# Kernel tuning notes

Measured on AMD Instinct MI355X. Metric: run time of the kernel, lower is better.

Reference implementation:

```python
import jax, jax.numpy as jnp
import numpy as np


def setup_inputs() -> dict:
    key = jax.random.key(0)
    ks = jax.random.split(key, 10)
    T, B, I, H, Z = 1024, 512, 128, 256, 1
    s = 0.1  # small init scale for stable recurrence
    return {
        "inputs": jax.random.normal(ks[0], (T, B, I), dtype=jnp.float32),
        "h0": jax.random.normal(ks[1], (B, H), dtype=jnp.float32) * s,
        "c0": jax.random.normal(ks[2], (B, H), dtype=jnp.float32) * s,
        "z0": jax.random.normal(ks[3], (B, Z), dtype=jnp.float32) * s,
        "W_ih": jax.random.normal(ks[4], (4 * H, I + Z), dtype=jnp.float32) * s,
        "W_hh": jax.random.normal(ks[5], (4 * H, H), dtype=jnp.float32) * s,
        "b_ih": jax.random.normal(ks[6], (4 * H,), dtype=jnp.float32) * s,
        "b_hh": jax.random.normal(ks[7], (4 * H,), dtype=jnp.float32) * s,
        "W_fc": jax.random.normal(ks[8], (Z, H), dtype=jnp.float32) * s,
        "b_fc": jax.random.normal(ks[9], (Z,), dtype=jnp.float32) * s,
    }


def reference(inputs, h0, c0, z0, W_ih, W_hh, b_ih, b_hh, W_fc, b_fc):
    def step(carry, x_t):
        h, c, z = carry
        xz = jnp.concatenate([x_t, z], axis=1)  # [B, I+Z]
        gates = xz @ W_ih.T + b_ih + h @ W_hh.T + b_hh  # [B, 4H]
        i_g, f_g, g_g, o_g = jnp.split(gates, 4, axis=1)  # torch gate order i,f,g,o
        i_g = jax.nn.sigmoid(i_g)
        f_g = jax.nn.sigmoid(f_g)
        g_g = jnp.tanh(g_g)
        o_g = jax.nn.sigmoid(o_g)
        c = f_g * c + i_g * g_g
        h = o_g * jnp.tanh(c)
        z = jnp.tanh(h @ W_fc.T + b_fc)  # [B, Z]
        return (h, c, z), z

    (h, c, _), outputs = jax.lax.scan(step, (h0, c0, z0), inputs)
    return outputs, h, c  # outputs: [T, B, Z]
```

## Files before the change

### kernel.cpp

```cpp
#include <hip/hip_runtime.h>
#include <hip/hip_bf16.h>
#include <stdint.h>

#define TT 1024
#define BB 512
#define II 128
#define HH 256
#define NKC 12
#define GSTR 132

typedef __attribute__((ext_vector_type(8))) short bf16x8;
typedef __attribute__((ext_vector_type(4))) float f32x4;
typedef __attribute__((ext_vector_type(4))) uint32_t u32x4;
typedef unsigned long long ull;

__device__ __forceinline__ float fsig(float x)  { return 1.0f / (1.0f + __expf(-x)); }
__device__ __forceinline__ float ftanh(float x) { return 1.0f - 2.0f / (__expf(2.0f * x) + 1.0f); }
__device__ __forceinline__ uint16_t f2bf(float f) {
    return __bfloat16_as_ushort(__float2bfloat16(f));
}
__device__ __forceinline__ float bf2lo(uint32_t w) { return __uint_as_float(w << 16); }
__device__ __forceinline__ float bf2hi(uint32_t w) { return __uint_as_float(w & 0xffff0000u); }

template<int DUAL>
__global__ __launch_bounds__(512, 1) void lstm_kernel(
    const float* __restrict__ x,
    const float* __restrict__ h0, const float* __restrict__ c0,
    const float* __restrict__ z0,
    const float* __restrict__ W_ih, const float* __restrict__ W_hh,
    const float* __restrict__ b_ih, const float* __restrict__ b_hh,
    const float* __restrict__ Wfc, const float* __restrict__ bfc,
    ull* __restrict__ hbF, ull* __restrict__ hbS,
    float* __restrict__ out)
{
    __shared__ __align__(16) uint16_t w_sh[NKC * 8 * 64 * 8];
    __shared__ __align__(16) uint16_t a_sh[NKC * 4 * 16 * 8];
    __shared__ float g_sh[16 * GSTR];
    __shared__ float zp_sh[2][8][16];

    const int tid  = threadIdx.x;
    const int lane = tid & 63, wv = tid >> 6;
    const int bid  = blockIdx.x;
    const int mm   = bid >> 3;
    const int role = mm & 7, grp = (bid & 7) * 4 + (mm >> 3);
    const int b0   = grp * 16;
    const int arow = tid >> 5, auu = tid & 31;
    const int u_g  = role * 32 + auu;
    const int xc   = (tid & 31) * 4;
    const int grole = wv, grow = (tid >> 2) & 15, gwq = tid & 3;

    #pragma unroll
    for (int i = 0; i < 12; ++i) {
        int eo = i * 512 + tid;
        int lane2 = eo & 63, knt = eo >> 6;
        int nt = knt & 7;
        int k0 = (knt >> 3) * 32 + (lane2 >> 4) * 8;
        int lc = nt * 16 + (lane2 & 15);
        int col = (lc >> 5) * 256 + role * 32 + (lc & 31);
        const float* src = (k0 < II) ? &W_ih[(size_t)col * (II + 1) + k0]
                                     : &W_hh[(size_t)col * HH + (k0 - II)];
        ushort4 lo, hi;
        lo.x = f2bf(src[0]); lo.y = f2bf(src[1]); lo.z = f2bf(src[2]); lo.w = f2bf(src[3]);
        hi.x = f2bf(src[4]); hi.y = f2bf(src[5]); hi.z = f2bf(src[6]); hi.w = f2bf(src[7]);
        *(ushort4*)&w_sh[eo * 8 + 0] = lo;
        *(ushort4*)&w_sh[eo * 8 + 4] = hi;
    }

    float bia[4], wzv[4];
    #pragma unroll
    for (int g = 0; g < 4; ++g) {
        int c = g * 256 + u_g;
        bia[g] = b_ih[c] + b_hh[c];
        wzv[g] = W_ih[(size_t)c * (II + 1) + II];
    }
    float wfc8[8];
    #pragma unroll
    for (int j = 0; j < 8; ++j) wfc8[j] = Wfc[grole * 32 + gwq * 8 + j];
    const float bfcs = bfc[0];
    const float z0r  = z0[b0 + arow];
    float c_r = c0[(size_t)(b0 + arow) * HH + u_g];

    {
        const float* hp = h0 + (size_t)(b0 + grow) * HH + grole * 32 + gwq * 8;
        uint4 pw;
        pw.x = (uint32_t)f2bf(hp[0]) | ((uint32_t)f2bf(hp[1]) << 16);
        pw.y = (uint32_t)f2bf(hp[2]) | ((uint32_t)f2bf(hp[3]) << 16);
        pw.z = (uint32_t)f2bf(hp[4]) | ((uint32_t)f2bf(hp[5]) << 16);
        pw.w = (uint32_t)f2bf(hp[6]) | ((uint32_t)f2bf(hp[7]) << 16);
        *(uint4*)&a_sh[(((4 + grole) * 4 + gwq) * 16 + grow) * 8] = pw;
    }
    {
        float4 xv = *(const float4*)&x[(size_t)(b0 + arow) * II + xc];
        int kcx = xc >> 5, gx = (xc >> 3) & 3, jx = xc & 7;
        ushort4 p;
        p.x = f2bf(xv.x); p.y = f2bf(xv.y); p.z = f2bf(xv.z); p.w = f2bf(xv.w);
        *(ushort4*)&a_sh[((kcx * 4 + gx) * 16 + arow) * 8 + jx] = p;
    }

    for (int t = 0; t <= TT; ++t) {
        float4 xn = make_float4(0.f, 0.f, 0.f, 0.f);
        if (t + 1 < TT)
            xn = *(const float4*)&x[(size_t)(t + 1) * (BB * II) + (size_t)(b0 + arow) * II + xc];

        if (t > 0) {
            const int par = (t - 1) & 1;
            const size_t gidx = ((((size_t)par * 32 + grp) * 8 + grole) * 16 + grow) * 16
                              + gwq * 4;
            const ull* pF = hbF + gidx;
            const ull* pS = hbS + gidx;
            u32x4 a0, a1;
            uint32_t it = 0;
            const uint32_t tt = (uint32_t)t;
            for (;;) {
                u32x4 s0, s1;
                if (DUAL) {
                    u32x4 f0, f1;
                    asm volatile(
                        "global_load_dwordx4 %0, %4, off sc0\n\t"
                        "global_load_dwordx4 %1, %4, off offset:16 sc0\n\t"
                        "global_load_dwordx4 %2, %5, off sc0 sc1\n\t"
                        "global_load_dwordx4 %3, %5, off offset:16 sc0 sc1\n\t"
                        "s_waitcnt vmcnt(0)"
                        : "=v"(f0), "=v"(f1), "=v"(s0), "=v"(s1)
                        : "v"(pF), "v"(pS) : "memory");
                    uint32_t mF = min(min(f0.y, f0.w), min(f1.y, f1.w));
                    if (mF >= tt) { a0 = f0; a1 = f1; break; }
                } else {
                    asm volatile(
                        "global_load_dwordx4 %0, %2, off sc0 sc1\n\t"
                        "global_load_dwordx4 %1, %2, off offset:16 sc0 sc1\n\t"
                        "s_waitcnt vmcnt(0)"
                        : "=v"(s0), "=v"(s1)
                        : "v"(pS) : "memory");
                }
                uint32_t mS = min(min(s0.y, s0.w), min(s1.y, s1.w));
                if (mS >= tt) { a0 = s0; a1 = s1; break; }
                __builtin_amdgcn_s_sleep(1);
                if (++it > (1u << 22)) { a0 = s0; a1 = s1; break; }
            }
            uint32_t w0 = a0.x, w1 = a0.z, w2 = a1.x, w3 = a1.z;
            uint4 pw; pw.x = w0; pw.y = w1; pw.z = w2; pw.w = w3;
            *(uint4*)&a_sh[(((4 + grole) * 4 + gwq) * 16 + grow) * 8] = pw;
            float p = bf2lo(w0) * wfc8[0] + bf2hi(w0) * wfc8[1]
                    + bf2lo(w1) * wfc8[2] + bf2hi(w1) * wfc8[3]
                    + bf2lo(w2) * wfc8[4] + bf2hi(w2) * wfc8[5]
                    + bf2lo(w3) * wfc8[6] + bf2hi(w3) * wfc8[7];
            p += __shfl_xor(p, 1, 64);
            p += __shfl_xor(p, 2, 64);
            if (gwq == 0) zp_sh[t & 1][grole][grow] = p;
        }
        __syncthreads();

        if (t == TT) {
            if (role == 0 && tid < 16) {
                float s = bfcs;
                #pragma unroll
                for (int r = 0; r < 8; ++r) s += zp_sh[TT & 1][r][tid];
                out[(size_t)(TT - 1) * BB + b0 + tid] = ftanh(s);
            }
            break;
        }

        f32x4 acc0 = {0.f, 0.f, 0.f, 0.f}, acc1 = {0.f, 0.f, 0.f, 0.f};
        #pragma unroll
        for (int kc = 0; kc < NKC; kc += 2) {
            bf16x8 a0 = *(const bf16x8*)&a_sh[((kc * 4 + (lane >> 4)) * 16 + (lane & 15)) * 8];
            bf16x8 bv0 = *(const bf16x8*)&w_sh[((kc * 8 + wv) * 64 + lane) * 8];
            acc0 = __builtin_amdgcn_mfma_f32_16x16x32_bf16(a0, bv0, acc0, 0, 0, 0);
            bf16x8 a1 = *(const bf16x8*)&a_sh[(((kc + 1) * 4 + (lane >> 4)) * 16 + (lane & 15)) * 8];
            bf16x8 bv1 = *(const bf16x8*)&w_sh[(((kc + 1) * 8 + wv) * 64 + lane) * 8];
            acc1 = __builtin_amdgcn_mfma_f32_16x16x32_bf16(a1, bv1, acc1, 0, 0, 0);
        }
        f32x4 acc = acc0 + acc1;
        {
            int r0 = (lane >> 4) * 4, cb = wv * 16 + (lane & 15);
            #pragma unroll
            for (int i = 0; i < 4; ++i) g_sh[(r0 + i) * GSTR + cb] = acc[i];
        }
        __syncthreads();

        {
            int kcx = xc >> 5, gx = (xc >> 3) & 3, jx = xc & 7;
            ushort4 p;
            p.x = f2bf(xn.x); p.y = f2bf(xn.y); p.z = f2bf(xn.z); p.w = f2bf(xn.w);
            *(ushort4*)&a_sh[((kcx * 4 + gx) * 16 + arow) * 8 + jx] = p;
        }

        float zp_;
        if (t == 0) {
            zp_ = z0r;
        } else {
            float s = bfcs;
            #pragma unroll
            for (int r = 0; r < 8; ++r) s += zp_sh[t & 1][r][arow];
            zp_ = ftanh(s);
            if (role == 0 && auu == 0)
                out[(size_t)(t - 1) * BB + b0 + arow] = zp_;
        }
        float gi = g_sh[arow * GSTR +      auu] + bia[0] + wzv[0] * zp_;
        float gf = g_sh[arow * GSTR + 32 + auu] + bia[1] + wzv[1] * zp_;
        float gg = g_sh[arow * GSTR + 64 + auu] + bia[2] + wzv[2] * zp_;
        float go = g_sh[arow * GSTR + 96 + auu] + bia[3] + wzv[3] * zp_;
        float ig = fsig(gi), fg = fsig(gf), gc = ftanh(gg), og = fsig(go);
        float cn = fg * c_r + ig * gc;
        c_r = cn;
        float hn = og * ftanh(cn);

        uint32_t hb16 = f2bf(hn);
        uint32_t nb = __shfl_down(hb16, 1, 64);
        if (!(auu & 1)) {
            ull q = ((ull)(uint32_t)(t + 1) << 32) | (ull)(hb16 | (nb << 16));
            size_t o = ((((size_t)(t & 1) * 32 + grp) * 8 + role) * 16 + arow) * 16
                     + (auu >> 1);
            if (DUAL)
                asm volatile("global_store_dwordx2 %0, %1, off sc0"
                             :: "v"(hbF + o), "v"(q) : "memory");
            asm volatile("global_store_dwordx2 %0, %1, off sc0 sc1"
                         :: "v"(hbS + o), "v"(q) : "memory");
        }

        if (t == TT - 1) {
            size_t ho = (size_t)TT * BB + (size_t)(b0 + arow) * HH + u_g;
            out[ho] = hn;
            out[ho + (size_t)BB * HH] = cn;
        }
    }
}

extern "C" void kernel_launch(void* const* d_in, const int* in_sizes, int n_in,
                              void* d_out, int out_size, void* d_ws, size_t ws_size,
                              hipStream_t stream) {
    const float* x    = (const float*)d_in[0];
    const float* h0   = (const float*)d_in[1];
    const float* c0   = (const float*)d_in[2];
    const float* z0   = (const float*)d_in[3];
    const float* W_ih = (const float*)d_in[4];
    const float* W_hh = (const float*)d_in[5];
    const float* b_ih = (const float*)d_in[6];
    const float* b_hh = (const float*)d_in[7];
    const float* Wfc  = (const float*)d_in[8];
    const float* bfc  = (const float*)d_in[9];
    float* out = (float*)d_out;

    const size_t COPY = (size_t)2 * 32 * 8 * 16 * 16 * 8;
    if (ws_size >= 2 * COPY) {
        ull* hbF = (ull*)d_ws;
        ull* hbS = (ull*)((char*)d_ws + COPY);
        hipMemsetAsync(d_ws, 0, 2 * COPY, stream);
        lstm_kernel<1><<<256, 512, 0, stream>>>(x, h0, c0, z0, W_ih, W_hh,
                                                b_ih, b_hh, Wfc, bfc,
                                                hbF, hbS, out);
    } else {
        ull* hbS = (ull*)d_ws;
        hipMemsetAsync(d_ws, 0, COPY, stream);
        lstm_kernel<0><<<256, 512, 0, stream>>>(x, h0, c0, z0, W_ih, W_hh,
                                                b_ih, b_hh, Wfc, bfc,
                                                hbS, hbS, out);
    }
}
```

Baseline: 2.405 ms.

## Keep weights in registers, write own h slice locally, poll faster copy first

Moves the per-block bf16 weight tile from LDS into registers so the MFMA loop reads only activations from shared memory. Each block now writes its own hidden-state slice and its FC partial sum straight into LDS and skips polling global memory for that slice. The DUAL polling loop tries the sc0-only buffer several times before falling back to the system-coherent copy, cutting the load traffic per poll. The cost is much higher register pressure (12 bf16x8 per thread), which could cause spills, and a lower timeout.

```diff
diff --git a/kernel.cpp b/kernel.cpp
--- a/kernel.cpp
+++ b/kernel.cpp
@@ -33,7 +33,6 @@
     ull* __restrict__ hbF, ull* __restrict__ hbS,
     float* __restrict__ out)
 {
-    __shared__ __align__(16) uint16_t w_sh[NKC * 8 * 64 * 8];
     __shared__ __align__(16) uint16_t a_sh[NKC * 4 * 16 * 8];
     __shared__ float g_sh[16 * GSTR];
     __shared__ float zp_sh[2][8][16];
@@ -49,21 +48,20 @@
     const int xc   = (tid & 31) * 4;
     const int grole = wv, grow = (tid >> 2) & 15, gwq = tid & 3;
 
-    #pragma unroll
-    for (int i = 0; i < 12; ++i) {
-        int eo = i * 512 + tid;
-        int lane2 = eo & 63, knt = eo >> 6;
-        int nt = knt & 7;
-        int k0 = (knt >> 3) * 32 + (lane2 >> 4) * 8;
-        int lc = nt * 16 + (lane2 & 15);
+    bf16x8 wreg[NKC];
+    {
+        int lc = wv * 16 + (lane & 15);
         int col = (lc >> 5) * 256 + role * 32 + (lc & 31);
-        const float* src = (k0 < II) ? &W_ih[(size_t)col * (II + 1) + k0]
-                                     : &W_hh[(size_t)col * HH + (k0 - II)];
-        ushort4 lo, hi;
-        lo.x = f2bf(src[0]); lo.y = f2bf(src[1]); lo.z = f2bf(src[2]); lo.w = f2bf(src[3]);
-        hi.x = f2bf(src[4]); hi.y = f2bf(src[5]); hi.z = f2bf(src[6]); hi.w = f2bf(src[7]);
-        *(ushort4*)&w_sh[eo * 8 + 0] = lo;
-        *(ushort4*)&w_sh[eo * 8 + 4] = hi;
+        #pragma unroll
+        for (int kc = 0; kc < NKC; ++kc) {
+            int k0 = kc * 32 + (lane >> 4) * 8;
+            const float* src = (k0 < II) ? &W_ih[(size_t)col * (II + 1) + k0]
+                                         : &W_hh[(size_t)col * HH + (k0 - II)];
+            bf16x8 wv8;
+            #pragma unroll
+            for (int j = 0; j < 8; ++j) wv8[j] = (short)f2bf(src[j]);
+            wreg[kc] = wv8;
+        }
     }
 
     float bia[4], wzv[4];
@@ -76,6 +74,7 @@
     float wfc8[8];
     #pragma unroll
     for (int j = 0; j < 8; ++j) wfc8[j] = Wfc[grole * 32 + gwq * 8 + j];
+    const float wfc  = Wfc[u_g];
     const float bfcs = bfc[0];
     const float z0r  = z0[b0 + arow];
     float c_r = c0[(size_t)(b0 + arow) * HH + u_g];
@@ -102,7 +101,7 @@
         if (t + 1 < TT)
             xn = *(const float4*)&x[(size_t)(t + 1) * (BB * II) + (size_t)(b0 + arow) * II + xc];
 
-        if (t > 0) {
+        if (t > 0 && grole != role) {
             const int par = (t - 1) & 1;
             const size_t gidx = ((((size_t)par * 32 + grp) * 8 + grole) * 16 + grow) * 16
                               + gwq * 4;
@@ -112,31 +111,27 @@
             uint32_t it = 0;
             const uint32_t tt = (uint32_t)t;
             for (;;) {
-                u32x4 s0, s1;
                 if (DUAL) {
                     u32x4 f0, f1;
                     asm volatile(
-                        "global_load_dwordx4 %0, %4, off sc0\n\t"
-                        "global_load_dwordx4 %1, %4, off offset:16 sc0\n\t"
-                        "global_load_dwordx4 %2, %5, off sc0 sc1\n\t"
-                        "global_load_dwordx4 %3, %5, off offset:16 sc0 sc1\n\t"
+                        "global_load_dwordx4 %0, %2, off sc0\n\t"
+                        "global_load_dwordx4 %1, %2, off offset:16 sc0\n\t"
                         "s_waitcnt vmcnt(0)"
-                        : "=v"(f0), "=v"(f1), "=v"(s0), "=v"(s1)
-                        : "v"(pF), "v"(pS) : "memory");
-                    uint32_t mF = min(min(f0.y, f0.w), min(f1.y, f1.w));
-                    if (mF >= tt) { a0 = f0; a1 = f1; break; }
-                } else {
-                    asm volatile(
-                        "global_load_dwordx4 %0, %2, off sc0 sc1\n\t"
-                        "global_load_dwordx4 %1, %2, off offset:16 sc0 sc1\n\t"
-                        "s_waitcnt vmcnt(0)"
-                        : "=v"(s0), "=v"(s1)
-                        : "v"(pS) : "memory");
+                        : "=&v"(f0), "=&v"(f1) : "v"(pF) : "memory");
+                    if (min(min(f0.y, f0.w), min(f1.y, f1.w)) >= tt) { a0 = f0; a1 = f1; break; }
+                    ++it;
+                    if ((it & 7) != 0) { __builtin_amdgcn_s_sleep(1); continue; }
                 }
-                uint32_t mS = min(min(s0.y, s0.w), min(s1.y, s1.w));
-                if (mS >= tt) { a0 = s0; a1 = s1; break; }
+                u32x4 s0, s1;
+                asm volatile(
+                    "global_load_dwordx4 %0, %2, off sc0 sc1\n\t"
+                    "global_load_dwordx4 %1, %2, off offset:16 sc0 sc1\n\t"
+                    "s_waitcnt vmcnt(0)"
+                    : "=&v"(s0), "=&v"(s1) : "v"(pS) : "memory");
+                if (min(min(s0.y, s0.w), min(s1.y, s1.w)) >= tt) { a0 = s0; a1 = s1; break; }
                 __builtin_amdgcn_s_sleep(1);
-                if (++it > (1u << 22)) { a0 = s0; a1 = s1; break; }
+                if (!DUAL) ++it;
+                if (it > (1u << 20)) { a0 = s0; a1 = s1; break; }
             }
             uint32_t w0 = a0.x, w1 = a0.z, w2 = a1.x, w3 = a1.z;
             uint4 pw; pw.x = w0; pw.y = w1; pw.z = w2; pw.w = w3;
@@ -165,11 +160,9 @@
         #pragma unroll
         for (int kc = 0; kc < NKC; kc += 2) {
             bf16x8 a0 = *(const bf16x8*)&a_sh[((kc * 4 + (lane >> 4)) * 16 + (lane & 15)) * 8];
-            bf16x8 bv0 = *(const bf16x8*)&w_sh[((kc * 8 + wv) * 64 + lane) * 8];
-            acc0 = __builtin_amdgcn_mfma_f32_16x16x32_bf16(a0, bv0, acc0, 0, 0, 0);
+            acc0 = __builtin_amdgcn_mfma_f32_16x16x32_bf16(a0, wreg[kc], acc0, 0, 0, 0);
             bf16x8 a1 = *(const bf16x8*)&a_sh[(((kc + 1) * 4 + (lane >> 4)) * 16 + (lane & 15)) * 8];
-            bf16x8 bv1 = *(const bf16x8*)&w_sh[(((kc + 1) * 8 + wv) * 64 + lane) * 8];
-            acc1 = __builtin_amdgcn_mfma_f32_16x16x32_bf16(a1, bv1, acc1, 0, 0, 0);
+            acc1 = __builtin_amdgcn_mfma_f32_16x16x32_bf16(a1, wreg[kc + 1], acc1, 0, 0, 0);
         }
         f32x4 acc = acc0 + acc1;
         {
@@ -209,7 +202,10 @@
         uint32_t hb16 = f2bf(hn);
         uint32_t nb = __shfl_down(hb16, 1, 64);
         if (!(auu & 1)) {
-            ull q = ((ull)(uint32_t)(t + 1) << 32) | (ull)(hb16 | (nb << 16));
+            uint32_t word = hb16 | (nb << 16);
+            *(uint32_t*)&a_sh[(((4 + role) * 4 + (auu >> 3)) * 16 + arow) * 8 + (auu & 7)]
+                = word;
+            ull q = ((ull)(uint32_t)(t + 1) << 32) | (ull)word;
             size_t o = ((((size_t)(t & 1) * 32 + grp) * 8 + role) * 16 + arow) * 16
                      + (auu >> 1);
             if (DUAL)
@@ -218,6 +214,10 @@
             asm volatile("global_store_dwordx2 %0, %1, off sc0 sc1"
                          :: "v"(hbS + o), "v"(q) : "memory");
         }
+        float pz = hn * wfc;
+        #pragma unroll
+        for (int off = 16; off >= 1; off >>= 1) pz += __shfl_xor(pz, off, 32);
+        if (auu == 0) zp_sh[(t + 1) & 1][role][arow] = pz;
 
         if (t == TT - 1) {
             size_t ho = (size_t)TT * BB + (size_t)(b0 + arow) * HH + u_g;
```

Measured after the change: 2.185 ms. 9.1% less time.
